# Kernel tuning notes

Measured on AMD Instinct MI355X. Metric: run time of the kernel, lower is better.

## Reference

```python
import jax, jax.numpy as jnp
import numpy as np

LEAK = 0.2
N = 1024      # nodes
C_IN = 64     # input channels
C_OUT = 64    # output channels
L = 2         # num_degrees -> L**2 = 4 spherical-harmonic index
LSQ = L * L
T = 15        # num_eret (edge retyping)


def setup_inputs() -> dict:
    key = jax.random.key(0)
    k1, k2, k3, k4 = jax.random.split(key, 4)
    x = jax.random.normal(k1, (N, C_IN), dtype=jnp.float32)
    adjacency = jax.random.normal(k2, (N, N, LSQ, T), dtype=jnp.float32)
    # learned params (truncated_normal init in keras; plain normal*0.05 here)
    W = jax.random.normal(k3, (C_IN, C_OUT, LSQ, T), dtype=jnp.float32) * 0.05
    W2 = jax.random.normal(k4, (C_IN, C_OUT), dtype=jnp.float32) * 0.05
    return {"x": x, "adjacency": adjacency, "W": W, "W2": W2}


def reference(x, adjacency, W, W2):
    # adjacency-weighted spherical-harmonic message passing:
    # temp[m, j] = sum_{n,i,l,t} adj[m,n,l,t] * x[n,i] * W[i,j,l,t]
    temp = jnp.einsum('mnlt,ni,ijlt->mj', adjacency, x, W)
    # skip / self connection
    temp = temp + jnp.einsum('ni,ij->nj', x, W2)
    # lrelu with leak 0.2 (use_bias=False)
    return jnp.maximum(temp, LEAK * temp)
```

## Files before the change

### kernel.cpp

```cpp
#include <hip/hip_runtime.h>
#include <hip/hip_bf16.h>
#include <stdint.h>

typedef __bf16 v8bf __attribute__((ext_vector_type(8)));
typedef float  v4f  __attribute__((ext_vector_type(4)));

#define LEAK 0.2f

static __device__ __forceinline__ unsigned short bf16rne(float f) {
    union { float f; uint32_t u; } v; v.f = f;
    return (unsigned short)((v.u + 0x7FFFu + ((v.u >> 16) & 1u)) >> 16);
}
static __device__ __forceinline__ float bf2f(unsigned short s) {
    union { uint32_t u; float f; } v; v.u = (uint32_t)s << 16; return v.f;
}
static __device__ __forceinline__ void gload16(const void* g, void* l) {
    __builtin_amdgcn_global_load_lds(
        (const __attribute__((address_space(1))) void*)g,
        (__attribute__((address_space(3))) void*)l, 16, 0, 0);
}

__global__ __launch_bounds__(256) void k1_ygemm(const float* __restrict__ x,
                                                const float* __restrict__ W,
                                                unsigned short* __restrict__ Yt) {
    __shared__ __align__(16) char lds[24576];
    const int blk = blockIdx.x;
    const int nt = blk / 60, ct = blk % 60;
    const int n0 = nt * 64, c0 = ct * 64;
    const int t = threadIdx.x;
    const int w = t >> 6, l = t & 63;
    const int lr = l & 15, lg = l >> 4;

#pragma unroll
    for (int k = 0; k < 4; ++k) {
        const int row = k * 16 + w * 4 + lg;
        const char* src = (const char*)(x + (size_t)(n0 + row) * 64)
                          + ((lr * 16) ^ ((row & 7) << 4));
        gload16(src, lds + k * 4096 + w * 1024);
    }
#pragma unroll
    for (int r = 0; r < 4; ++r) {
        const int q = t + (r << 8);
        const int i = q >> 4;
        const int c4 = (q & 15) << 2;
        const float4 v = *reinterpret_cast<const float4*>(W + (size_t)i * 3840 + c0 + c4);
        const unsigned short b0 = bf16rne(v.x), b1 = bf16rne(v.y);
        const unsigned short b2 = bf16rne(v.z), b3 = bf16rne(v.w);
#pragma unroll
        for (int e = 0; e < 4; ++e) {
            const int c = c4 + e;
            const unsigned short bv = (e == 0) ? b0 : (e == 1) ? b1 : (e == 2) ? b2 : b3;
            *(unsigned short*)(lds + 16384 + c * 128 + ((i * 2) ^ ((c & 7) << 4))) = bv;
        }
    }
    __syncthreads();

    v4f acc[4];
#pragma unroll
    for (int jt = 0; jt < 4; ++jt) acc[jt] = (v4f){0.f, 0.f, 0.f, 0.f};

    const int ar = 16 * w + lr;
    const int sa = (ar & 7) << 4;

#pragma unroll
    for (int s = 0; s < 2; ++s) {
        const int Xf = s * 128 + lg * 32;
        const float4 x0 = *reinterpret_cast<const float4*>(lds + ar * 256 + (Xf ^ sa));
        const float4 x1 = *reinterpret_cast<const float4*>(lds + ar * 256 + ((Xf + 16) ^ sa));
        v8bf af;
        af[0] = (__bf16)x0.x; af[1] = (__bf16)x0.y;
        af[2] = (__bf16)x0.z; af[3] = (__bf16)x0.w;
        af[4] = (__bf16)x1.x; af[5] = (__bf16)x1.y;
        af[6] = (__bf16)x1.z; af[7] = (__bf16)x1.w;

#pragma unroll
        for (int jt = 0; jt < 4; ++jt) {
            const int c = jt * 16 + lr;
            const v8bf bf = *reinterpret_cast<const v8bf*>(
                lds + 16384 + c * 128 + ((s * 64 + lg * 16) ^ ((c & 7) << 4)));
            acc[jt] = __builtin_amdgcn_mfma_f32_16x16x32_bf16(af, bf, acc[jt], 0, 0, 0);
        }
    }

#pragma unroll
    for (int jt = 0; jt < 4; ++jt) {
#pragma unroll
        for (int r = 0; r < 4; ++r) {
            const int n = n0 + 16 * w + lg * 4 + r;
            const int c = c0 + jt * 16 + lr;
            const int j = c / 60, lt = c % 60;
            Yt[j * 61440 + n * 60 + lt] = bf16rne(acc[jt][r]);
        }
    }
}

__global__ __launch_bounds__(256) void k2_main(const float* __restrict__ adj,
                                               const unsigned short* __restrict__ Yt,
                                               unsigned short* __restrict__ partial) {
    __shared__ __align__(16) char lds[73728];
    const int blk = blockIdx.x;
    const int mt = blk >> 5, ks = blk & 31;
    const int m0 = mt * 64;
    const long kc0 = (long)ks * 1920;
    const int t = threadIdx.x;
    const int w = t >> 6, l = t & 63;
    const int lr = l & 15, lg = l >> 4;

    const char* srcA[4];
    const char* srcB[2];
#pragma unroll
    for (int k = 0; k < 4; ++k) {
        const int row = k * 16 + w * 4 + lg;
        srcA[k] = (const char*)(adj + (size_t)(m0 + row) * 61440 + kc0)
                  + ((lr * 16) ^ ((row & 7) << 4));
    }
#pragma unroll
    for (int k = 0; k < 2; ++k) {
        const int row = k * 32 + w * 8 + (l >> 3);
        srcB[k] = (const char*)(Yt + (size_t)row * 61440 + kc0)
                  + (((l & 7) * 16) ^ ((row & 7) << 4));
    }

#define STAGE(bs, s) do {                                                      \
        char* ab_ = lds + (bs) * 16384;                                        \
        char* bb_ = lds + 49152 + (bs) * 8192;                                 \
        _Pragma("unroll")                                                      \
        for (int k_ = 0; k_ < 4; ++k_)                                         \
            gload16(srcA[k_] + (size_t)(s) * 256, ab_ + k_ * 4096 + w * 1024); \
        _Pragma("unroll")                                                      \
        for (int k_ = 0; k_ < 2; ++k_)                                         \
            gload16(srcB[k_] + (size_t)(s) * 128, bb_ + k_ * 4096 + w * 1024); \
    } while (0)

    v4f acc[4];
#pragma unroll
    for (int jt = 0; jt < 4; ++jt) acc[jt] = (v4f){0.f, 0.f, 0.f, 0.f};

    const int ar = 16 * w + lr;
    const int sa = (ar & 7) << 4;

    STAGE(0, 0);
    STAGE(1, 1);
    int bs = 2, bc = 0;

#pragma unroll 1
    for (int i = 0; i < 30; ++i) {
        if (i < 29) { asm volatile("s_waitcnt vmcnt(6)" ::: "memory"); }
        else        { asm volatile("s_waitcnt vmcnt(0)" ::: "memory"); }
        __builtin_amdgcn_s_barrier();
        asm volatile("" ::: "memory");
        if (i < 28) STAGE(bs, i + 2);

        const char* ab = lds + bc * 16384;
        const char* bb = lds + 49152 + bc * 8192;
        v8bf af[2];
#pragma unroll
        for (int ss = 0; ss < 2; ++ss) {
            const int Xf = ss * 128 + lg * 32;
            const float4 x0 = *reinterpret_cast<const float4*>(ab + ar * 256 + (Xf ^ sa));
            const float4 x1 = *reinterpret_cast<const float4*>(ab + ar * 256 + ((Xf + 16) ^ sa));
            v8bf f;
            f[0] = (__bf16)x0.x; f[1] = (__bf16)x0.y;
            f[2] = (__bf16)x0.z; f[3] = (__bf16)x0.w;
            f[4] = (__bf16)x1.x; f[5] = (__bf16)x1.y;
            f[6] = (__bf16)x1.z; f[7] = (__bf16)x1.w;
            af[ss] = f;
        }
#pragma unroll
        for (int jt = 0; jt < 4; ++jt) {
            const int br = 16 * jt + lr;
            const int sb = (br & 7) << 4;
            const v8bf b0 = *reinterpret_cast<const v8bf*>(bb + br * 128 + ((lg * 16) ^ sb));
            const v8bf b1 = *reinterpret_cast<const v8bf*>(bb + br * 128 + ((64 + lg * 16) ^ sb));
            acc[jt] = __builtin_amdgcn_mfma_f32_16x16x32_bf16(af[0], b0, acc[jt], 0, 0, 0);
            acc[jt] = __builtin_amdgcn_mfma_f32_16x16x32_bf16(af[1], b1, acc[jt], 0, 0, 0);
        }

        bs = (bs == 2) ? 0 : bs + 1;
        bc = (bc == 2) ? 0 : bc + 1;
    }
#undef STAGE

    unsigned short* const p = partial + (size_t)ks * 65536;
#pragma unroll
    for (int jt = 0; jt < 4; ++jt) {
#pragma unroll
        for (int r = 0; r < 4; ++r) {
            const int m = m0 + 16 * w + lg * 4 + r;
            const int j = jt * 16 + lr;
            p[m * 64 + j] = bf16rne(acc[jt][r]);
        }
    }
}

__global__ __launch_bounds__(256) void k3_epi(const unsigned short* __restrict__ partial,
                                              const float* __restrict__ x,
                                              const float* __restrict__ W2,
                                              float* __restrict__ out) {
    const int idx = blockIdx.x * 256 + threadIdx.x;
    const int m = idx >> 4;
    const int j0 = (idx & 15) * 4;

    float a0 = 0.f, a1 = 0.f, a2 = 0.f, a3 = 0.f;
#pragma unroll 8
    for (int sp = 0; sp < 32; ++sp) {
        const uint2 a = *reinterpret_cast<const uint2*>(
            partial + (size_t)sp * 65536 + m * 64 + j0);
        a0 += bf2f((unsigned short)(a.x & 0xffff));
        a1 += bf2f((unsigned short)(a.x >> 16));
        a2 += bf2f((unsigned short)(a.y & 0xffff));
        a3 += bf2f((unsigned short)(a.y >> 16));
    }

    const float* xrow = x + m * 64;
#pragma unroll 8
    for (int i = 0; i < 64; ++i) {
        const float xv = xrow[i];
        const float4 wv = *reinterpret_cast<const float4*>(W2 + i * 64 + j0);
        a0 += xv * wv.x; a1 += xv * wv.y;
        a2 += xv * wv.z; a3 += xv * wv.w;
    }

    float4 o;
    o.x = fmaxf(a0, LEAK * a0);
    o.y = fmaxf(a1, LEAK * a1);
    o.z = fmaxf(a2, LEAK * a2);
    o.w = fmaxf(a3, LEAK * a3);
    *reinterpret_cast<float4*>(out + m * 64 + j0) = o;
}

extern "C" void kernel_launch(void* const* d_in, const int* in_sizes, int n_in,
                              void* d_out, int out_size, void* d_ws, size_t ws_size,
                              hipStream_t stream) {
    const float* x   = (const float*)d_in[0];
    const float* adj = (const float*)d_in[1];
    const float* W   = (const float*)d_in[2];
    const float* W2  = (const float*)d_in[3];
    float* out = (float*)d_out;

    char* ws = (char*)d_ws;
    unsigned short* Yt      = (unsigned short*)ws;
    unsigned short* partial = (unsigned short*)(ws + 7864320);

    k1_ygemm<<<960, 256, 0, stream>>>(x, W, Yt);
    k2_main <<<512, 256, 0, stream>>>(adj, Yt, partial);
    k3_epi  <<<64,  256, 0, stream>>>(partial, x, W2, out);
}
```

Measured before the change: 54.75 us.

## Deepen k2 pipeline to six smaller stages and widen epilogue grid

The main GEMM kernel's K-step is halved (32 floats of adjacency per stage instead of 64), and the LDS ring grows from three to six buffers, with five stages prefetched ahead. The main loop is fully unrolled in groups of six with constant buffer indices and an explicit drain tail. This aims to keep more global loads in flight and remove dynamic buffer-index arithmetic, at the cost of twice as many barriers per tile. The epilogue kernel now gives each thread one output element, spread over four times as many blocks, to raise parallelism in the reduction.

New measurement: 60.37 us. +10.3%, slower.

```diff
diff --git a/kernel.cpp b/kernel.cpp
--- a/kernel.cpp
+++ b/kernel.cpp
@@ -106,30 +106,30 @@
     const int w = t >> 6, l = t & 63;
     const int lr = l & 15, lg = l >> 4;
 
-    const char* srcA[4];
-    const char* srcB[2];
-#pragma unroll
-    for (int k = 0; k < 4; ++k) {
-        const int row = k * 16 + w * 4 + lg;
-        srcA[k] = (const char*)(adj + (size_t)(m0 + row) * 61440 + kc0)
-                  + ((lr * 16) ^ ((row & 7) << 4));
-    }
-#pragma unroll
-    for (int k = 0; k < 2; ++k) {
-        const int row = k * 32 + w * 8 + (l >> 3);
-        srcB[k] = (const char*)(Yt + (size_t)row * 61440 + kc0)
-                  + (((l & 7) * 16) ^ ((row & 7) << 4));
-    }
-
-#define STAGE(bs, s) do {                                                      \
-        char* ab_ = lds + (bs) * 16384;                                        \
-        char* bb_ = lds + 49152 + (bs) * 8192;                                 \
-        _Pragma("unroll")                                                      \
-        for (int k_ = 0; k_ < 4; ++k_)                                         \
-            gload16(srcA[k_] + (size_t)(s) * 256, ab_ + k_ * 4096 + w * 1024); \
-        _Pragma("unroll")                                                      \
-        for (int k_ = 0; k_ < 2; ++k_)                                         \
-            gload16(srcB[k_] + (size_t)(s) * 128, bb_ + k_ * 4096 + w * 1024); \
+    const char* srcA0;
+    const char* srcA1;
+    {
+        const int r0 = w * 8 + (l >> 3);
+        const int r1 = 32 + r0;
+        srcA0 = (const char*)(adj + (size_t)(m0 + r0) * 61440 + kc0)
+                + (((l & 7) * 16) ^ ((r0 & 7) << 4));
+        srcA1 = (const char*)(adj + (size_t)(m0 + r1) * 61440 + kc0)
+                + (((l & 7) * 16) ^ ((r1 & 7) << 4));
+    }
+    const char* srcB;
+    {
+        const int sinner = ((l & 7) << 4) ^ (((l >> 3) & 7) << 4);
+        const int brow = 2 * (w * 8 + (l >> 3)) + ((sinner >> 6) & 1);
+        const int bkb = sinner & 63;
+        srcB = (const char*)(Yt + (size_t)brow * 61440 + kc0) + bkb;
+    }
+
+#define STAGE(bs, s) do {                                            \
+        char* ab_ = lds + (bs) * 8192;                               \
+        char* bb_ = lds + 49152 + (bs) * 4096;                       \
+        gload16(srcA0 + (size_t)(s) * 128, ab_ + w * 1024);          \
+        gload16(srcA1 + (size_t)(s) * 128, ab_ + 4096 + w * 1024);   \
+        gload16(srcB  + (size_t)(s) * 64,  bb_ + w * 1024);          \
     } while (0)
 
     v4f acc[4];
@@ -139,46 +139,56 @@
     const int ar = 16 * w + lr;
     const int sa = (ar & 7) << 4;
 
-    STAGE(0, 0);
-    STAGE(1, 1);
-    int bs = 2, bc = 0;
+#define COMPUTE(bc) do {                                                            \
+        const char* ab = lds + (bc) * 8192;                                         \
+        const char* bb = lds + 49152 + (bc) * 4096;                                 \
+        const float4 x0 = *reinterpret_cast<const float4*>(                         \
+            ab + ar * 128 + ((lg * 32) ^ sa));                                      \
+        const float4 x1 = *reinterpret_cast<const float4*>(                         \
+            ab + ar * 128 + ((lg * 32 + 16) ^ sa));                                 \
+        v8bf af;                                                                    \
+        af[0] = (__bf16)x0.x; af[1] = (__bf16)x0.y;                                 \
+        af[2] = (__bf16)x0.z; af[3] = (__bf16)x0.w;                                 \
+        af[4] = (__bf16)x1.x; af[5] = (__bf16)x1.y;                                 \
+        af[6] = (__bf16)x1.z; af[7] = (__bf16)x1.w;                                 \
+        _Pragma("unroll")                                                           \
+        for (int jt = 0; jt < 4; ++jt) {                                            \
+            const int br = jt * 16 + lr;                                            \
+            const v8bf bf = *reinterpret_cast<const v8bf*>(                         \
+                bb + (br >> 1) * 128 +                                              \
+                ((((br & 1) * 64) + lg * 16) ^ (((br >> 1) & 7) << 4)));            \
+            acc[jt] = __builtin_amdgcn_mfma_f32_16x16x32_bf16(af, bf, acc[jt],      \
+                                                              0, 0, 0);             \
+        }                                                                           \
+    } while (0)
+
+#define WAITB(N) do {                                               \
+        asm volatile("s_waitcnt vmcnt(" #N ")" ::: "memory");       \
+        __builtin_amdgcn_s_barrier();                               \
+        asm volatile("" ::: "memory");                              \
+    } while (0)
+
+    STAGE(0, 0); STAGE(1, 1); STAGE(2, 2); STAGE(3, 3); STAGE(4, 4);
 
 #pragma unroll 1
-    for (int i = 0; i < 30; ++i) {
-        if (i < 29) { asm volatile("s_waitcnt vmcnt(6)" ::: "memory"); }
-        else        { asm volatile("s_waitcnt vmcnt(0)" ::: "memory"); }
-        __builtin_amdgcn_s_barrier();
-        asm volatile("" ::: "memory");
-        if (i < 28) STAGE(bs, i + 2);
-
-        const char* ab = lds + bc * 16384;
-        const char* bb = lds + 49152 + bc * 8192;
-        v8bf af[2];
-#pragma unroll
-        for (int ss = 0; ss < 2; ++ss) {
-            const int Xf = ss * 128 + lg * 32;
-            const float4 x0 = *reinterpret_cast<const float4*>(ab + ar * 256 + (Xf ^ sa));
-            const float4 x1 = *reinterpret_cast<const float4*>(ab + ar * 256 + ((Xf + 16) ^ sa));
-            v8bf f;
-            f[0] = (__bf16)x0.x; f[1] = (__bf16)x0.y;
-            f[2] = (__bf16)x0.z; f[3] = (__bf16)x0.w;
-            f[4] = (__bf16)x1.x; f[5] = (__bf16)x1.y;
-            f[6] = (__bf16)x1.z; f[7] = (__bf16)x1.w;
-            af[ss] = f;
-        }
-#pragma unroll
-        for (int jt = 0; jt < 4; ++jt) {
-            const int br = 16 * jt + lr;
-            const int sb = (br & 7) << 4;
-            const v8bf b0 = *reinterpret_cast<const v8bf*>(bb + br * 128 + ((lg * 16) ^ sb));
-            const v8bf b1 = *reinterpret_cast<const v8bf*>(bb + br * 128 + ((64 + lg * 16) ^ sb));
-            acc[jt] = __builtin_amdgcn_mfma_f32_16x16x32_bf16(af[0], b0, acc[jt], 0, 0, 0);
-            acc[jt] = __builtin_amdgcn_mfma_f32_16x16x32_bf16(af[1], b1, acc[jt], 0, 0, 0);
-        }
-
-        bs = (bs == 2) ? 0 : bs + 1;
-        bc = (bc == 2) ? 0 : bc + 1;
-    }
+    for (int ii = 0; ii < 9; ++ii) {
+        const int ib = ii * 6;
+#pragma unroll
+        for (int u = 0; u < 6; ++u) {
+            WAITB(12);
+            STAGE((u + 5) % 6, ib + u + 5);
+            COMPUTE(u);
+        }
+    }
+    WAITB(12); STAGE(5, 59); COMPUTE(0);
+    WAITB(12); COMPUTE(1);
+    WAITB(9);  COMPUTE(2);
+    WAITB(6);  COMPUTE(3);
+    WAITB(3);  COMPUTE(4);
+    WAITB(0);  COMPUTE(5);
+
+#undef WAITB
+#undef COMPUTE
 #undef STAGE
 
     unsigned short* const p = partial + (size_t)ks * 65536;
@@ -198,35 +208,17 @@
                                               const float* __restrict__ W2,
                                               float* __restrict__ out) {
     const int idx = blockIdx.x * 256 + threadIdx.x;
-    const int m = idx >> 4;
-    const int j0 = (idx & 15) * 4;
-
-    float a0 = 0.f, a1 = 0.f, a2 = 0.f, a3 = 0.f;
+    const int m = idx >> 6, j = idx & 63;
+
+    float s = 0.f;
 #pragma unroll 8
-    for (int sp = 0; sp < 32; ++sp) {
-        const uint2 a = *reinterpret_cast<const uint2*>(
-            partial + (size_t)sp * 65536 + m * 64 + j0);
-        a0 += bf2f((unsigned short)(a.x & 0xffff));
-        a1 += bf2f((unsigned short)(a.x >> 16));
-        a2 += bf2f((unsigned short)(a.y & 0xffff));
-        a3 += bf2f((unsigned short)(a.y >> 16));
-    }
+    for (int sp = 0; sp < 32; ++sp) s += bf2f(partial[(size_t)sp * 65536 + idx]);
 
     const float* xrow = x + m * 64;
 #pragma unroll 8
-    for (int i = 0; i < 64; ++i) {
-        const float xv = xrow[i];
-        const float4 wv = *reinterpret_cast<const float4*>(W2 + i * 64 + j0);
-        a0 += xv * wv.x; a1 += xv * wv.y;
-        a2 += xv * wv.z; a3 += xv * wv.w;
-    }
-
-    float4 o;
-    o.x = fmaxf(a0, LEAK * a0);
-    o.y = fmaxf(a1, LEAK * a1);
-    o.z = fmaxf(a2, LEAK * a2);
-    o.w = fmaxf(a3, LEAK * a3);
-    *reinterpret_cast<float4*>(out + m * 64 + j0) = o;
+    for (int i = 0; i < 64; ++i) s += xrow[i] * W2[i * 64 + j];
+
+    out[idx] = fmaxf(s, LEAK * s);
 }
 
 extern "C" void kernel_launch(void* const* d_in, const int* in_sizes, int n_in,
@@ -244,5 +236,5 @@
 
     k1_ygemm<<<960, 256, 0, stream>>>(x, W, Yt);
     k2_main <<<512, 256, 0, stream>>>(adj, Yt, partial);
-    k3_epi  <<<64,  256, 0, stream>>>(partial, x, W2, out);
-}
+    k3_epi  <<<256, 256, 0, stream>>>(partial, x, W2, out);
+}
```

## Stage adjacency through registers with bf16 conversion before LDS to cut LDS footprint

Applied to the files above, without the earlier changes.

The fp32 adjacency tile now goes through registers instead of direct global-to-LDS loads. It is converted to bf16 before being written to LDS, which halves the A buffer size and drops the per-iteration conversion at fragment read time. LDS use falls from 72KB to 40KB and launch bounds ask for 4 blocks per CU, so the memory-bound main GEMM can run at higher occupancy. The cost is more VGPRs for the in-flight register buffers, an extra lgkmcnt wait before each barrier, and a more complex, fully unrolled pipeline schedule.

Measured after the change: 66.40 us. +21.3%, slower.

```diff
diff --git a/kernel.cpp b/kernel.cpp
--- a/kernel.cpp
+++ b/kernel.cpp
@@ -94,10 +94,10 @@
     }
 }
 
-__global__ __launch_bounds__(256) void k2_main(const float* __restrict__ adj,
-                                               const unsigned short* __restrict__ Yt,
-                                               unsigned short* __restrict__ partial) {
-    __shared__ __align__(16) char lds[73728];
+__global__ __launch_bounds__(256, 4) void k2_main(const float* __restrict__ adj,
+                                                  const unsigned short* __restrict__ Yt,
+                                                  unsigned short* __restrict__ partial) {
+    __shared__ __align__(16) char lds[40960];
     const int blk = blockIdx.x;
     const int mt = blk >> 5, ks = blk & 31;
     const int m0 = mt * 64;
@@ -106,14 +106,13 @@
     const int w = t >> 6, l = t & 63;
     const int lr = l & 15, lg = l >> 4;
 
-    const char* srcA[4];
+    const float* srcA[4];
+#pragma unroll
+    for (int k = 0; k < 4; ++k)
+        srcA[k] = adj + (size_t)(m0 + k * 16 + w * 4 + lg) * 61440 + kc0 + lr * 4;
+    const int aw_off = (w * 4 + lg) * 128 + ((lr * 8) ^ (((w * 4 + lg) & 7) << 4));
+
     const char* srcB[2];
-#pragma unroll
-    for (int k = 0; k < 4; ++k) {
-        const int row = k * 16 + w * 4 + lg;
-        srcA[k] = (const char*)(adj + (size_t)(m0 + row) * 61440 + kc0)
-                  + ((lr * 16) ^ ((row & 7) << 4));
-    }
 #pragma unroll
     for (int k = 0; k < 2; ++k) {
         const int row = k * 32 + w * 8 + (l >> 3);
@@ -121,15 +120,31 @@
                   + (((l & 7) * 16) ^ ((row & 7) << 4));
     }
 
-#define STAGE(bs, s) do {                                                      \
-        char* ab_ = lds + (bs) * 16384;                                        \
-        char* bb_ = lds + 49152 + (bs) * 8192;                                 \
+    float4 areg[2][4];
+
+#define ISSUE_A(pa, s) do {                                                    \
         _Pragma("unroll")                                                      \
         for (int k_ = 0; k_ < 4; ++k_)                                         \
-            gload16(srcA[k_] + (size_t)(s) * 256, ab_ + k_ * 4096 + w * 1024); \
+            areg[pa][k_] = *reinterpret_cast<const float4*>(                   \
+                srcA[k_] + (size_t)(s) * 64);                                  \
+    } while (0)
+
+#define ISSUE_B(pbn, s) do {                                                   \
+        char* bb_ = lds + 16384 + (pbn) * 8192;                                \
+        gload16(srcB[0] + (size_t)(s) * 128, bb_ + w * 1024);                  \
+        gload16(srcB[1] + (size_t)(s) * 128, bb_ + 4096 + w * 1024);           \
+    } while (0)
+
+#define WRITE_A(pa) do {                                                       \
+        char* ab_ = lds + (pa) * 8192;                                         \
         _Pragma("unroll")                                                      \
-        for (int k_ = 0; k_ < 2; ++k_)                                         \
-            gload16(srcB[k_] + (size_t)(s) * 128, bb_ + k_ * 4096 + w * 1024); \
+        for (int k_ = 0; k_ < 4; ++k_) {                                       \
+            const float4 v_ = areg[pa][k_];                                    \
+            uint2 p_;                                                          \
+            p_.x = (uint32_t)bf16rne(v_.x) | ((uint32_t)bf16rne(v_.y) << 16);  \
+            p_.y = (uint32_t)bf16rne(v_.z) | ((uint32_t)bf16rne(v_.w) << 16);  \
+            *reinterpret_cast<uint2*>(ab_ + k_ * 2048 + aw_off) = p_;          \
+        }                                                                      \
     } while (0)
 
     v4f acc[4];
@@ -139,47 +154,67 @@
     const int ar = 16 * w + lr;
     const int sa = (ar & 7) << 4;
 
-    STAGE(0, 0);
-    STAGE(1, 1);
-    int bs = 2, bc = 0;
+#define COMPUTE(pa, pb) do {                                                   \
+        const char* ab = lds + (pa) * 8192;                                    \
+        const char* bb = lds + 16384 + (pb) * 8192;                            \
+        const v8bf af0 = *reinterpret_cast<const v8bf*>(                       \
+            ab + ar * 128 + ((lg * 16) ^ sa));                                 \
+        const v8bf af1 = *reinterpret_cast<const v8bf*>(                       \
+            ab + ar * 128 + ((64 + lg * 16) ^ sa));                            \
+        _Pragma("unroll")                                                      \
+        for (int jt = 0; jt < 4; ++jt) {                                       \
+            const int br = jt * 16 + lr;                                       \
+            const int sb = (br & 7) << 4;                                      \
+            const v8bf b0 = *reinterpret_cast<const v8bf*>(                    \
+                bb + br * 128 + ((lg * 16) ^ sb));                             \
+            const v8bf b1 = *reinterpret_cast<const v8bf*>(                    \
+                bb + br * 128 + ((64 + lg * 16) ^ sb));                        \
+            acc[jt] = __builtin_amdgcn_mfma_f32_16x16x32_bf16(af0, b0,         \
+                                                              acc[jt], 0,0,0); \
+            acc[jt] = __builtin_amdgcn_mfma_f32_16x16x32_bf16(af1, b1,         \
+                                                              acc[jt], 0,0,0); \
+        }                                                                      \
+    } while (0)
+
+#define STEP(pa, pb, pbn, snext, doissue) do {                                 \
+        asm volatile("s_waitcnt vmcnt(6)" ::: "memory");                       \
+        WRITE_A(pa);                                                           \
+        if (doissue) ISSUE_A(pa, snext);                                       \
+        asm volatile("s_waitcnt lgkmcnt(0)" ::: "memory");                     \
+        __builtin_amdgcn_s_barrier();                                          \
+        asm volatile("" ::: "memory");                                         \
+        if (doissue) ISSUE_B(pbn, snext);                                      \
+        COMPUTE(pa, pb);                                                       \
+    } while (0)
+
+    ISSUE_A(0, 0); ISSUE_B(0, 0); ISSUE_A(1, 1); ISSUE_B(1, 1);
 
 #pragma unroll 1
-    for (int i = 0; i < 30; ++i) {
-        if (i < 29) { asm volatile("s_waitcnt vmcnt(6)" ::: "memory"); }
-        else        { asm volatile("s_waitcnt vmcnt(0)" ::: "memory"); }
+    for (int ii = 0; ii < 4; ++ii) {
+        const int ib = ii * 6;
+#pragma unroll
+        for (int u = 0; u < 6; ++u)
+            STEP(u & 1, u % 3, (u + 2) % 3, ib + u + 2, true);
+    }
+    STEP(0, 0, 2, 26, true);
+    STEP(1, 1, 0, 27, true);
+    STEP(0, 2, 1, 28, true);
+    STEP(1, 0, 2, 29, true);
+    STEP(0, 1, 0, 0, false);
+    {
+        asm volatile("s_waitcnt vmcnt(0)" ::: "memory");
+        WRITE_A(1);
+        asm volatile("s_waitcnt lgkmcnt(0)" ::: "memory");
         __builtin_amdgcn_s_barrier();
         asm volatile("" ::: "memory");
-        if (i < 28) STAGE(bs, i + 2);
-
-        const char* ab = lds + bc * 16384;
-        const char* bb = lds + 49152 + bc * 8192;
-        v8bf af[2];
-#pragma unroll
-        for (int ss = 0; ss < 2; ++ss) {
-            const int Xf = ss * 128 + lg * 32;
-            const float4 x0 = *reinterpret_cast<const float4*>(ab + ar * 256 + (Xf ^ sa));
-            const float4 x1 = *reinterpret_cast<const float4*>(ab + ar * 256 + ((Xf + 16) ^ sa));
-            v8bf f;
-            f[0] = (__bf16)x0.x; f[1] = (__bf16)x0.y;
-            f[2] = (__bf16)x0.z; f[3] = (__bf16)x0.w;
-            f[4] = (__bf16)x1.x; f[5] = (__bf16)x1.y;
-            f[6] = (__bf16)x1.z; f[7] = (__bf16)x1.w;
-            af[ss] = f;
-        }
-#pragma unroll
-        for (int jt = 0; jt < 4; ++jt) {
-            const int br = 16 * jt + lr;
-            const int sb = (br & 7) << 4;
-            const v8bf b0 = *reinterpret_cast<const v8bf*>(bb + br * 128 + ((lg * 16) ^ sb));
-            const v8bf b1 = *reinterpret_cast<const v8bf*>(bb + br * 128 + ((64 + lg * 16) ^ sb));
-            acc[jt] = __builtin_amdgcn_mfma_f32_16x16x32_bf16(af[0], b0, acc[jt], 0, 0, 0);
-            acc[jt] = __builtin_amdgcn_mfma_f32_16x16x32_bf16(af[1], b1, acc[jt], 0, 0, 0);
-        }
-
-        bs = (bs == 2) ? 0 : bs + 1;
-        bc = (bc == 2) ? 0 : bc + 1;
-    }
-#undef STAGE
+        COMPUTE(1, 2);
+    }
+
+#undef STEP
+#undef COMPUTE
+#undef WRITE_A
+#undef ISSUE_B
+#undef ISSUE_A
 
     unsigned short* const p = partial + (size_t)ks * 65536;
 #pragma unroll
```
